# Kernel optimization log

Measured on AMD Instinct MI355X. Metric: run time of the kernel, lower is better.

The kernel has to match this reference:

```python
import jax, jax.numpy as jnp
import numpy as np

B, N, NB, C, CZ = 4, 1024, 32, 384, 128
EPS = 1e-6


def setup_inputs() -> dict:
    key = jax.random.key(0)
    k1, k2, k3, k4, k5 = jax.random.split(key, 5)
    s_i = jax.random.normal(k1, (B, N, C), dtype=jnp.float32)
    s_ij = jax.random.normal(k2, (B, N, NB, C), dtype=jnp.float32)
    m_ij = jnp.ones((B, N, NB), dtype=jnp.float32)
    z_ij = jax.random.normal(k3, (B, N, NB, CZ), dtype=jnp.float32)
    W_s = jax.random.normal(k4, (C, C), dtype=jnp.float32) / np.sqrt(C)
    W_z = jax.random.normal(k5, (CZ, C), dtype=jnp.float32) / np.sqrt(CZ)
    gamma = jnp.ones((C,), dtype=jnp.float32)
    beta = jnp.zeros((C,), dtype=jnp.float32)
    return {"s_i": s_i, "s_ij": s_ij, "m_ij": m_ij, "z_ij": z_ij,
            "W_s": W_s, "W_z": W_z, "gamma": gamma, "beta": beta}


def reference(s_i, s_ij, m_ij, z_ij, W_s, W_z, gamma, beta):
    # Dense projection of neighbor single act: (B,N,n,C) @ (C,C)
    s_proj = jnp.einsum('bnkc,cd->bnkd', s_ij, W_s)
    # subtract center single act
    diff = s_proj - s_i[..., None, :]
    # gate by projected pair act: (B,N,n,Cz) @ (Cz,C)
    gate = jnp.einsum('bnkz,zd->bnkd', z_ij, W_z)
    msg = diff * gate
    # masked sum over neighbor axis
    s_new = jnp.sum(msg * m_ij[..., None], axis=-2)  # (B,N,C)
    # layernorm over last axis
    mu = jnp.mean(s_new, axis=-1, keepdims=True)
    var = jnp.mean(jnp.square(s_new - mu), axis=-1, keepdims=True)
    s_new = (s_new - mu) * jax.lax.rsqrt(var + EPS) * gamma + beta
    return s_new
```

## Files before the change

kernel.cpp:

```cpp
#include <hip/hip_runtime.h>
#include <hip/hip_bf16.h>

#define B_ 4
#define N_ 1024
#define NB_ 32
#define C_ 384
#define CZ_ 128
#define NSITES (B_ * N_)
#define EPSV 1e-6f
#define PAD 40
#define SPB 4
#define MROWS 128
#define THREADS 512

typedef unsigned short u16;
typedef unsigned int u32;
typedef __bf16 bf16x8 __attribute__((ext_vector_type(8)));
typedef float f32x4 __attribute__((ext_vector_type(4)));

__device__ __forceinline__ u16 f2bf(float f) {
    return __builtin_bit_cast(u16, __float2bfloat16(f));
}
__device__ __forceinline__ float bfbits2f(u16 u) {
    union { float f; u32 i; } x;
    x.i = ((u32)u) << 16;
    return x.f;
}

__global__ void prep_weights(const float* __restrict__ Ws, const float* __restrict__ Wz,
                             u16* __restrict__ Wts, u16* __restrict__ Wtz) {
    int idx = blockIdx.x * 256 + threadIdx.x;
    if (idx < C_ * C_) {
        int d = idx / C_, c = idx % C_;
        Wts[idx] = f2bf(Ws[c * C_ + d]);
    } else {
        int j = idx - C_ * C_;
        if (j < C_ * CZ_) {
            int d = j / CZ_, z = j % CZ_;
            Wtz[j] = f2bf(Wz[z * C_ + d]);
        }
    }
}

struct Stage {
    uint4 w0, w1, w2;
    float4 a0, a1;
};

__device__ __forceinline__ void issue_stage(Stage& st, const u16* __restrict__ Wt, int kdim,
                                            const float* __restrict__ A, long rowbase,
                                            int kc, int tid) {
    int ar = tid >> 2, ag = tid & 3;
    const float* src = A + (rowbase + ar) * (long)kdim + kc + ag * 8;
    st.a0 = *reinterpret_cast<const float4*>(src);
    st.a1 = *reinterpret_cast<const float4*>(src + 4);
    int s = tid;
    st.w0 = *reinterpret_cast<const uint4*>(Wt + (s >> 2) * kdim + kc + (s & 3) * 8);
    s = tid + 512;
    st.w1 = *reinterpret_cast<const uint4*>(Wt + (s >> 2) * kdim + kc + (s & 3) * 8);
    s = tid + 1024;
    st.w2 = *reinterpret_cast<const uint4*>(Wt + (s >> 2) * kdim + kc + (s & 3) * 8);
}

__device__ __forceinline__ void commit_stage(const Stage& st, u16* ldsW, u16* ldsA, int tid) {
    int s = tid;
    *reinterpret_cast<uint4*>(&ldsW[(s >> 2) * PAD + (s & 3) * 8]) = st.w0;
    s = tid + 512;
    *reinterpret_cast<uint4*>(&ldsW[(s >> 2) * PAD + (s & 3) * 8]) = st.w1;
    s = tid + 1024;
    *reinterpret_cast<uint4*>(&ldsW[(s >> 2) * PAD + (s & 3) * 8]) = st.w2;
    int ar = tid >> 2, ag = tid & 3;
    uint4 h;
    h.x = ((u32)f2bf(st.a0.y) << 16) | f2bf(st.a0.x);
    h.y = ((u32)f2bf(st.a0.w) << 16) | f2bf(st.a0.z);
    h.z = ((u32)f2bf(st.a1.y) << 16) | f2bf(st.a1.x);
    h.w = ((u32)f2bf(st.a1.w) << 16) | f2bf(st.a1.z);
    *reinterpret_cast<uint4*>(&ldsA[ar * PAD + ag * 8]) = h;
}

__device__ __forceinline__ void compute_chunk(const u16* ldsW, const u16* ldsA,
                                              f32x4 (&acc)[4][6],
                                              int mg, int colbase, int ln, int q) {
    bf16x8 a[4];
    #pragma unroll
    for (int mt = 0; mt < 4; ++mt)
        a[mt] = *reinterpret_cast<const bf16x8*>(&ldsA[(mg * 64 + mt * 16 + ln) * PAD + q * 8]);
    #pragma unroll
    for (int nt = 0; nt < 6; ++nt) {
        bf16x8 b = *reinterpret_cast<const bf16x8*>(&ldsW[(colbase + nt * 16 + ln) * PAD + q * 8]);
        #pragma unroll
        for (int mt = 0; mt < 4; ++mt)
            acc[mt][nt] = __builtin_amdgcn_mfma_f32_16x16x32_bf16(a[mt], b, acc[mt][nt], 0, 0, 0);
    }
}

__global__ __launch_bounds__(THREADS, 2)
void fused_msg_kernel(const float* __restrict__ s_i,
                      const float* __restrict__ s_ij,
                      const float* __restrict__ m_ij,
                      const float* __restrict__ z_ij,
                      const u16* __restrict__ Wts,
                      const u16* __restrict__ Wtz,
                      const float* __restrict__ gamma,
                      const float* __restrict__ beta,
                      float* __restrict__ out) {
    __shared__ u16 ldsW[C_ * PAD];
    __shared__ u16 ldsA[2][MROWS * PAD];
    __shared__ float lds_si[SPB * C_];
    __shared__ float lds_m[MROWS];
    __shared__ float lds_snew[SPB * C_];

    const int tid = threadIdx.x;
    const int wave = tid >> 6;
    const int lane = tid & 63;
    const int q = lane >> 4;
    const int ln = lane & 15;
    const int mg = wave >> 2;
    const int colbase = (wave & 3) * 96;

    const int site0 = blockIdx.x * SPB;
    const long rowbase = (long)site0 * NB_;

    for (int i = tid; i < SPB * C_; i += THREADS)
        lds_si[i] = s_i[(long)site0 * C_ + i];
    if (tid < MROWS) lds_m[tid] = m_ij[rowbase + tid];

    const f32x4 ZERO = {0.f, 0.f, 0.f, 0.f};
    f32x4 acc[4][6];
    #pragma unroll
    for (int mt = 0; mt < 4; ++mt)
        #pragma unroll
        for (int nt = 0; nt < 6; ++nt)
            acc[mt][nt] = ZERO;

    Stage st;

    {
        const int NK = CZ_ / 32;
        issue_stage(st, Wtz, CZ_, z_ij, rowbase, 0, tid);
        commit_stage(st, ldsW, ldsA[0], tid);
        __syncthreads();
        #pragma unroll 2
        for (int c = 0; c < NK; ++c) {
            if (c + 1 < NK) issue_stage(st, Wtz, CZ_, z_ij, rowbase, (c + 1) * 32, tid);
            compute_chunk(ldsW, ldsA[c & 1], acc, mg, colbase, ln, q);
            __syncthreads();
            if (c + 1 < NK) {
                commit_stage(st, ldsW, ldsA[(c + 1) & 1], tid);
                __syncthreads();
            }
        }
    }

    u32 gateb[4][6][2];
    #pragma unroll
    for (int mt = 0; mt < 4; ++mt) {
        int rb = mg * 64 + mt * 16 + q * 4;
        float m0 = lds_m[rb + 0];
        float m1 = lds_m[rb + 1];
        float m2 = lds_m[rb + 2];
        float m3 = lds_m[rb + 3];
        #pragma unroll
        for (int nt = 0; nt < 6; ++nt) {
            gateb[mt][nt][0] = ((u32)f2bf(acc[mt][nt][1] * m1) << 16) | f2bf(acc[mt][nt][0] * m0);
            gateb[mt][nt][1] = ((u32)f2bf(acc[mt][nt][3] * m3) << 16) | f2bf(acc[mt][nt][2] * m2);
            acc[mt][nt] = ZERO;
        }
    }

    {
        const int NK = C_ / 32;
        issue_stage(st, Wts, C_, s_ij, rowbase, 0, tid);
        commit_stage(st, ldsW, ldsA[0], tid);
        __syncthreads();
        #pragma unroll 2
        for (int c = 0; c < NK; ++c) {
            if (c + 1 < NK) issue_stage(st, Wts, C_, s_ij, rowbase, (c + 1) * 32, tid);
            compute_chunk(ldsW, ldsA[c & 1], acc, mg, colbase, ln, q);
            __syncthreads();
            if (c + 1 < NK) {
                commit_stage(st, ldsW, ldsA[(c + 1) & 1], tid);
                __syncthreads();
            }
        }
    }

    #pragma unroll
    for (int sl = 0; sl < 2; ++sl) {
        int site = mg * 2 + sl;
        #pragma unroll
        for (int nt = 0; nt < 6; ++nt) {
            int col = colbase + nt * 16 + ln;
            float si = lds_si[site * C_ + col];
            float p = 0.f;
            #pragma unroll
            for (int mh = 0; mh < 2; ++mh) {
                int mt = sl * 2 + mh;
                #pragma unroll
                for (int r = 0; r < 4; ++r) {
                    float g = bfbits2f((u16)(gateb[mt][nt][r >> 1] >> ((r & 1) * 16)));
                    p += (acc[mt][nt][r] - si) * g;
                }
            }
            p += __shfl_xor(p, 16, 64);
            p += __shfl_xor(p, 32, 64);
            if (q == 0) lds_snew[site * C_ + col] = p;
        }
    }
    __syncthreads();

    if (wave < SPB) {
        const int site = wave;
        float v[6];
        float sum = 0.f, sumsq = 0.f;
        #pragma unroll
        for (int i = 0; i < 6; ++i) {
            v[i] = lds_snew[site * C_ + lane + i * 64];
            sum += v[i];
            sumsq += v[i] * v[i];
        }
        #pragma unroll
        for (int off = 32; off >= 1; off >>= 1) {
            sum += __shfl_xor(sum, off, 64);
            sumsq += __shfl_xor(sumsq, off, 64);
        }
        float mu = sum * (1.f / C_);
        float var = sumsq * (1.f / C_) - mu * mu;
        float rs = rsqrtf(var + EPSV);
        #pragma unroll
        for (int i = 0; i < 6; ++i) {
            int col = lane + i * 64;
            out[(long)(site0 + site) * C_ + col] = (v[i] - mu) * rs * gamma[col] + beta[col];
        }
    }
}

extern "C" void kernel_launch(void* const* d_in, const int* in_sizes, int n_in,
                              void* d_out, int out_size, void* d_ws, size_t ws_size,
                              hipStream_t stream) {
    (void)in_sizes; (void)n_in; (void)out_size; (void)ws_size;
    const float* s_i   = (const float*)d_in[0];
    const float* s_ij  = (const float*)d_in[1];
    const float* m_ij  = (const float*)d_in[2];
    const float* z_ij  = (const float*)d_in[3];
    const float* W_s   = (const float*)d_in[4];
    const float* W_z   = (const float*)d_in[5];
    const float* gamma = (const float*)d_in[6];
    const float* beta  = (const float*)d_in[7];
    float* out = (float*)d_out;

    u16* wts = (u16*)d_ws;
    u16* wtz = wts + C_ * C_;

    int prep_elems = C_ * C_ + C_ * CZ_;
    prep_weights<<<(prep_elems + 255) / 256, 256, 0, stream>>>(W_s, W_z, wts, wtz);
    fused_msg_kernel<<<NSITES / SPB, THREADS, 0, stream>>>(s_i, s_ij, m_ij, z_ij, wts, wtz,
                                                           gamma, beta, out);
}
```

Baseline: 447.3 us.

## Halve sites per block, double-buffer weight tiles, raise occupancy to four blocks

Each block now handles 2 sites (64 neighbor rows) instead of 4, which halves the accumulator registers per wave, and the launch bound rises to 4 blocks per SM. The weight tile in LDS is now double-buffered, so each K-chunk needs one barrier instead of two. The mask is read per lane and broadcast with shuffles, and s_i is read straight from global memory instead of being staged in LDS. The cost is that every block reloads the full weight matrices for half as many rows, doubling weight traffic per site.

```diff
diff --git a/kernel.cpp b/kernel.cpp
--- a/kernel.cpp
+++ b/kernel.cpp
@@ -9,8 +9,8 @@
 #define NSITES (B_ * N_)
 #define EPSV 1e-6f
 #define PAD 40
-#define SPB 4
-#define MROWS 128
+#define SPB 2
+#define MR 64
 #define THREADS 512
 
 typedef unsigned short u16;
@@ -20,6 +20,9 @@
 
 __device__ __forceinline__ u16 f2bf(float f) {
     return __builtin_bit_cast(u16, __float2bfloat16(f));
+}
+__device__ __forceinline__ u32 pk2(float lo, float hi) {
+    return ((u32)f2bf(hi) << 16) | f2bf(lo);
 }
 __device__ __forceinline__ float bfbits2f(u16 u) {
     union { float f; u32 i; } x;
@@ -42,59 +45,7 @@
     }
 }
 
-struct Stage {
-    uint4 w0, w1, w2;
-    float4 a0, a1;
-};
-
-__device__ __forceinline__ void issue_stage(Stage& st, const u16* __restrict__ Wt, int kdim,
-                                            const float* __restrict__ A, long rowbase,
-                                            int kc, int tid) {
-    int ar = tid >> 2, ag = tid & 3;
-    const float* src = A + (rowbase + ar) * (long)kdim + kc + ag * 8;
-    st.a0 = *reinterpret_cast<const float4*>(src);
-    st.a1 = *reinterpret_cast<const float4*>(src + 4);
-    int s = tid;
-    st.w0 = *reinterpret_cast<const uint4*>(Wt + (s >> 2) * kdim + kc + (s & 3) * 8);
-    s = tid + 512;
-    st.w1 = *reinterpret_cast<const uint4*>(Wt + (s >> 2) * kdim + kc + (s & 3) * 8);
-    s = tid + 1024;
-    st.w2 = *reinterpret_cast<const uint4*>(Wt + (s >> 2) * kdim + kc + (s & 3) * 8);
-}
-
-__device__ __forceinline__ void commit_stage(const Stage& st, u16* ldsW, u16* ldsA, int tid) {
-    int s = tid;
-    *reinterpret_cast<uint4*>(&ldsW[(s >> 2) * PAD + (s & 3) * 8]) = st.w0;
-    s = tid + 512;
-    *reinterpret_cast<uint4*>(&ldsW[(s >> 2) * PAD + (s & 3) * 8]) = st.w1;
-    s = tid + 1024;
-    *reinterpret_cast<uint4*>(&ldsW[(s >> 2) * PAD + (s & 3) * 8]) = st.w2;
-    int ar = tid >> 2, ag = tid & 3;
-    uint4 h;
-    h.x = ((u32)f2bf(st.a0.y) << 16) | f2bf(st.a0.x);
-    h.y = ((u32)f2bf(st.a0.w) << 16) | f2bf(st.a0.z);
-    h.z = ((u32)f2bf(st.a1.y) << 16) | f2bf(st.a1.x);
-    h.w = ((u32)f2bf(st.a1.w) << 16) | f2bf(st.a1.z);
-    *reinterpret_cast<uint4*>(&ldsA[ar * PAD + ag * 8]) = h;
-}
-
-__device__ __forceinline__ void compute_chunk(const u16* ldsW, const u16* ldsA,
-                                              f32x4 (&acc)[4][6],
-                                              int mg, int colbase, int ln, int q) {
-    bf16x8 a[4];
-    #pragma unroll
-    for (int mt = 0; mt < 4; ++mt)
-        a[mt] = *reinterpret_cast<const bf16x8*>(&ldsA[(mg * 64 + mt * 16 + ln) * PAD + q * 8]);
-    #pragma unroll
-    for (int nt = 0; nt < 6; ++nt) {
-        bf16x8 b = *reinterpret_cast<const bf16x8*>(&ldsW[(colbase + nt * 16 + ln) * PAD + q * 8]);
-        #pragma unroll
-        for (int mt = 0; mt < 4; ++mt)
-            acc[mt][nt] = __builtin_amdgcn_mfma_f32_16x16x32_bf16(a[mt], b, acc[mt][nt], 0, 0, 0);
-    }
-}
-
-__global__ __launch_bounds__(THREADS, 2)
+__global__ __launch_bounds__(THREADS, 4)
 void fused_msg_kernel(const float* __restrict__ s_i,
                       const float* __restrict__ s_ij,
                       const float* __restrict__ m_ij,
@@ -104,10 +55,8 @@
                       const float* __restrict__ gamma,
                       const float* __restrict__ beta,
                       float* __restrict__ out) {
-    __shared__ u16 ldsW[C_ * PAD];
-    __shared__ u16 ldsA[2][MROWS * PAD];
-    __shared__ float lds_si[SPB * C_];
-    __shared__ float lds_m[MROWS];
+    __shared__ u16 ldsW[2][C_ * PAD];
+    __shared__ u16 ldsA[2][MR * PAD];
     __shared__ float lds_snew[SPB * C_];
 
     const int tid = threadIdx.x;
@@ -116,96 +65,163 @@
     const int q = lane >> 4;
     const int ln = lane & 15;
     const int mg = wave >> 2;
-    const int colbase = (wave & 3) * 96;
+    const int cb = (wave & 3) * 96;
 
     const int site0 = blockIdx.x * SPB;
     const long rowbase = (long)site0 * NB_;
 
-    for (int i = tid; i < SPB * C_; i += THREADS)
-        lds_si[i] = s_i[(long)site0 * C_ + i];
-    if (tid < MROWS) lds_m[tid] = m_ij[rowbase + tid];
+    const int arow = tid >> 3, aseg = tid & 7;
+    const int wrow = tid >> 2, wseg = tid & 3;
+    const int la_w = arow * PAD + aseg * 4;
+    const int lw_w = wrow * PAD + wseg * 8;
+
+    const float mv = m_ij[rowbase + lane];
 
     const f32x4 ZERO = {0.f, 0.f, 0.f, 0.f};
-    f32x4 acc[4][6];
+    f32x4 acc[2][6];
     #pragma unroll
-    for (int mt = 0; mt < 4; ++mt)
+    for (int mt = 0; mt < 2; ++mt)
         #pragma unroll
         for (int nt = 0; nt < 6; ++nt)
             acc[mt][nt] = ZERO;
 
-    Stage st;
+    float4 ra;
+    uint4 rw0, rw1, rw2;
 
     {
-        const int NK = CZ_ / 32;
-        issue_stage(st, Wtz, CZ_, z_ij, rowbase, 0, tid);
-        commit_stage(st, ldsW, ldsA[0], tid);
+        const int kd = CZ_;
+        const float* ap = z_ij + (rowbase + arow) * kd + aseg * 4;
+        const u16* wp = Wtz + wrow * kd + wseg * 8;
+        const int ws1 = 128 * kd, ws2 = 256 * kd;
+
+        ra = *reinterpret_cast<const float4*>(ap);
+        rw0 = *reinterpret_cast<const uint4*>(wp);
+        rw1 = *reinterpret_cast<const uint4*>(wp + ws1);
+        rw2 = *reinterpret_cast<const uint4*>(wp + ws2);
+        ap += 32; wp += 32;
+        {
+            uint2 a2 = {pk2(ra.x, ra.y), pk2(ra.z, ra.w)};
+            *reinterpret_cast<uint2*>(&ldsA[0][la_w]) = a2;
+            *reinterpret_cast<uint4*>(&ldsW[0][lw_w]) = rw0;
+            *reinterpret_cast<uint4*>(&ldsW[0][lw_w + 128 * PAD]) = rw1;
+            *reinterpret_cast<uint4*>(&ldsW[0][lw_w + 256 * PAD]) = rw2;
+        }
         __syncthreads();
+
         #pragma unroll 2
-        for (int c = 0; c < NK; ++c) {
-            if (c + 1 < NK) issue_stage(st, Wtz, CZ_, z_ij, rowbase, (c + 1) * 32, tid);
-            compute_chunk(ldsW, ldsA[c & 1], acc, mg, colbase, ln, q);
+        for (int c = 0; c < 4; ++c) {
+            if (c + 1 < 4) {
+                ra = *reinterpret_cast<const float4*>(ap);
+                rw0 = *reinterpret_cast<const uint4*>(wp);
+                rw1 = *reinterpret_cast<const uint4*>(wp + ws1);
+                rw2 = *reinterpret_cast<const uint4*>(wp + ws2);
+                ap += 32; wp += 32;
+            }
+            const u16* lA = ldsA[c & 1];
+            const u16* lW = ldsW[c & 1];
+            bf16x8 a0 = *reinterpret_cast<const bf16x8*>(&lA[(mg * 32 + ln) * PAD + q * 8]);
+            bf16x8 a1 = *reinterpret_cast<const bf16x8*>(&lA[(mg * 32 + 16 + ln) * PAD + q * 8]);
+            #pragma unroll
+            for (int nt = 0; nt < 6; ++nt) {
+                bf16x8 b = *reinterpret_cast<const bf16x8*>(&lW[(cb + nt * 16 + ln) * PAD + q * 8]);
+                acc[0][nt] = __builtin_amdgcn_mfma_f32_16x16x32_bf16(a0, b, acc[0][nt], 0, 0, 0);
+                acc[1][nt] = __builtin_amdgcn_mfma_f32_16x16x32_bf16(a1, b, acc[1][nt], 0, 0, 0);
+            }
+            if (c + 1 < 4) {
+                int nb = (c + 1) & 1;
+                uint2 a2 = {pk2(ra.x, ra.y), pk2(ra.z, ra.w)};
+                *reinterpret_cast<uint2*>(&ldsA[nb][la_w]) = a2;
+                *reinterpret_cast<uint4*>(&ldsW[nb][lw_w]) = rw0;
+                *reinterpret_cast<uint4*>(&ldsW[nb][lw_w + 128 * PAD]) = rw1;
+                *reinterpret_cast<uint4*>(&ldsW[nb][lw_w + 256 * PAD]) = rw2;
+            }
             __syncthreads();
-            if (c + 1 < NK) {
-                commit_stage(st, ldsW, ldsA[(c + 1) & 1], tid);
-                __syncthreads();
-            }
-        }
-    }
-
-    u32 gateb[4][6][2];
+        }
+    }
+
+    u32 gateb[2][6][2];
     #pragma unroll
-    for (int mt = 0; mt < 4; ++mt) {
-        int rb = mg * 64 + mt * 16 + q * 4;
-        float m0 = lds_m[rb + 0];
-        float m1 = lds_m[rb + 1];
-        float m2 = lds_m[rb + 2];
-        float m3 = lds_m[rb + 3];
+    for (int mt = 0; mt < 2; ++mt) {
+        int rb = mg * 32 + mt * 16 + q * 4;
+        float m0 = __shfl(mv, rb + 0, 64);
+        float m1 = __shfl(mv, rb + 1, 64);
+        float m2 = __shfl(mv, rb + 2, 64);
+        float m3 = __shfl(mv, rb + 3, 64);
         #pragma unroll
         for (int nt = 0; nt < 6; ++nt) {
-            gateb[mt][nt][0] = ((u32)f2bf(acc[mt][nt][1] * m1) << 16) | f2bf(acc[mt][nt][0] * m0);
-            gateb[mt][nt][1] = ((u32)f2bf(acc[mt][nt][3] * m3) << 16) | f2bf(acc[mt][nt][2] * m2);
+            gateb[mt][nt][0] = pk2(acc[mt][nt][0] * m0, acc[mt][nt][1] * m1);
+            gateb[mt][nt][1] = pk2(acc[mt][nt][2] * m2, acc[mt][nt][3] * m3);
             acc[mt][nt] = ZERO;
         }
     }
 
     {
-        const int NK = C_ / 32;
-        issue_stage(st, Wts, C_, s_ij, rowbase, 0, tid);
-        commit_stage(st, ldsW, ldsA[0], tid);
+        const int kd = C_;
+        const float* ap = s_ij + (rowbase + arow) * kd + aseg * 4;
+        const u16* wp = Wts + wrow * kd + wseg * 8;
+        const int ws1 = 128 * kd, ws2 = 256 * kd;
+
+        ra = *reinterpret_cast<const float4*>(ap);
+        rw0 = *reinterpret_cast<const uint4*>(wp);
+        rw1 = *reinterpret_cast<const uint4*>(wp + ws1);
+        rw2 = *reinterpret_cast<const uint4*>(wp + ws2);
+        ap += 32; wp += 32;
+        {
+            uint2 a2 = {pk2(ra.x, ra.y), pk2(ra.z, ra.w)};
+            *reinterpret_cast<uint2*>(&ldsA[0][la_w]) = a2;
+            *reinterpret_cast<uint4*>(&ldsW[0][lw_w]) = rw0;
+            *reinterpret_cast<uint4*>(&ldsW[0][lw_w + 128 * PAD]) = rw1;
+            *reinterpret_cast<uint4*>(&ldsW[0][lw_w + 256 * PAD]) = rw2;
+        }
         __syncthreads();
+
         #pragma unroll 2
-        for (int c = 0; c < NK; ++c) {
-            if (c + 1 < NK) issue_stage(st, Wts, C_, s_ij, rowbase, (c + 1) * 32, tid);
-            compute_chunk(ldsW, ldsA[c & 1], acc, mg, colbase, ln, q);
+        for (int c = 0; c < 12; ++c) {
+            if (c + 1 < 12) {
+                ra = *reinterpret_cast<const float4*>(ap);
+                rw0 = *reinterpret_cast<const uint4*>(wp);
+                rw1 = *reinterpret_cast<const uint4*>(wp + ws1);
+                rw2 = *reinterpret_cast<const uint4*>(wp + ws2);
+                ap += 32; wp += 32;
+            }
+            const u16* lA = ldsA[c & 1];
+            const u16* lW = ldsW[c & 1];
+            bf16x8 a0 = *reinterpret_cast<const bf16x8*>(&lA[(mg * 32 + ln) * PAD + q * 8]);
+            bf16x8 a1 = *reinterpret_cast<const bf16x8*>(&lA[(mg * 32 + 16 + ln) * PAD + q * 8]);
+            #pragma unroll
+            for (int nt = 0; nt < 6; ++nt) {
+                bf16x8 b = *reinterpret_cast<const bf16x8*>(&lW[(cb + nt * 16 + ln) * PAD + q * 8]);
+                acc[0][nt] = __builtin_amdgcn_mfma_f32_16x16x32_bf16(a0, b, acc[0][nt], 0, 0, 0);
+                acc[1][nt] = __builtin_amdgcn_mfma_f32_16x16x32_bf16(a1, b, acc[1][nt], 0, 0, 0);
+            }
+            if (c + 1 < 12) {
+                int nb = (c + 1) & 1;
+                uint2 a2 = {pk2(ra.x, ra.y), pk2(ra.z, ra.w)};
+                *reinterpret_cast<uint2*>(&ldsA[nb][la_w]) = a2;
+                *reinterpret_cast<uint4*>(&ldsW[nb][lw_w]) = rw0;
+                *reinterpret_cast<uint4*>(&ldsW[nb][lw_w + 128 * PAD]) = rw1;
+                *reinterpret_cast<uint4*>(&ldsW[nb][lw_w + 256 * PAD]) = rw2;
+            }
             __syncthreads();
-            if (c + 1 < NK) {
-                commit_stage(st, ldsW, ldsA[(c + 1) & 1], tid);
-                __syncthreads();
-            }
         }
     }
 
     #pragma unroll
-    for (int sl = 0; sl < 2; ++sl) {
-        int site = mg * 2 + sl;
-        #pragma unroll
-        for (int nt = 0; nt < 6; ++nt) {
-            int col = colbase + nt * 16 + ln;
-            float si = lds_si[site * C_ + col];
-            float p = 0.f;
+    for (int nt = 0; nt < 6; ++nt) {
+        int col = cb + nt * 16 + ln;
+        float si = s_i[(long)(site0 + mg) * C_ + col];
+        float p = 0.f;
+        #pragma unroll
+        for (int mt = 0; mt < 2; ++mt) {
             #pragma unroll
-            for (int mh = 0; mh < 2; ++mh) {
-                int mt = sl * 2 + mh;
-                #pragma unroll
-                for (int r = 0; r < 4; ++r) {
-                    float g = bfbits2f((u16)(gateb[mt][nt][r >> 1] >> ((r & 1) * 16)));
-                    p += (acc[mt][nt][r] - si) * g;
-                }
-            }
-            p += __shfl_xor(p, 16, 64);
-            p += __shfl_xor(p, 32, 64);
-            if (q == 0) lds_snew[site * C_ + col] = p;
-        }
+            for (int r = 0; r < 4; ++r) {
+                float g = bfbits2f((u16)(gateb[mt][nt][r >> 1] >> ((r & 1) * 16)));
+                p += (acc[mt][nt][r] - si) * g;
+            }
+        }
+        p += __shfl_xor(p, 16, 64);
+        p += __shfl_xor(p, 32, 64);
+        if (q == 0) lds_snew[mg * C_ + col] = p;
     }
     __syncthreads();
 
```

After: 438.7 us. Within noise of the previous version (-1.9%).
